# Performance work log

Measured on AMD Instinct MI355X. Metric: run time of the kernel, lower is better.

Reference implementation:

```python
import jax, jax.numpy as jnp
import numpy as np

N, C, A = 8192, 1000, 2048


def setup_inputs() -> dict:
    key = jax.random.key(0)
    k1, k2, k3, k4, k5, k6 = jax.random.split(key, 6)
    return {
        "fc": jax.random.normal(k1, (C, A), dtype=jnp.float32) * 0.02,
        "features_source": jax.random.normal(k2, (N, A), dtype=jnp.float32),
        "y_s": jax.random.normal(k3, (N, C), dtype=jnp.float32),
        "labels_source": jax.random.randint(k4, (N,), 0, C),
        "ratio": jnp.ones((1,), dtype=jnp.float32),
        "weights": jax.random.uniform(k5, (C,), dtype=jnp.float32, minval=0.5, maxval=1.5),
        "cv": jax.random.uniform(k6, (C, A), dtype=jnp.float32),
    }


def _metasaug_logits(fc, y_s, labels, cv, ratio):
    # sigma2[i,j] = ratio * sum_a (W[j,a] - W[y_i,a])^2 * cv[y_i,a]
    # expand the square -> three GEMM/reduction terms, avoiding the NxCxA tensor
    cv_y = cv[labels]            # (N, A)
    W_y = fc[labels]             # (N, A)
    term1 = cv_y @ (fc * fc).T                                   # (N, C)
    term2 = jnp.sum((W_y * W_y) * cv_y, axis=-1, keepdims=True)  # (N, 1)
    term3 = (W_y * cv_y) @ fc.T                                  # (N, C)
    sigma2 = ratio * (term1 + term2 - 2.0 * term3)
    return y_s + 0.5 * sigma2


def reference(fc, features_source, y_s, labels_source, ratio, weights, cv):
    # mode != 'update' path: augmented logits + class-weighted cross entropy
    aug_y = _metasaug_logits(fc, y_s, labels_source, cv, ratio)
    logp = jax.nn.log_softmax(aug_y, axis=-1)
    nll = -jnp.take_along_axis(logp, labels_source[:, None], axis=1)[:, 0]  # (N,)
    w = weights[labels_source]
    # torch weighted CE with mean reduction divides by sum of per-sample weights
    return jnp.sum(w * nll) / jnp.sum(w)
```

## Files before the change

### kernel.cpp

```cpp
#include <hip/hip_runtime.h>
#include <hip/hip_fp16.h>

#define N_SAMP 8192
#define C_CLS  1000
#define A_DIM  2048
#define KDIM   4096
#define CP     1024
#define ZSPLIT 8

typedef _Float16 half8 __attribute__((ext_vector_type(8)));
typedef _Float16 half4 __attribute__((ext_vector_type(4)));
typedef float    f32x4 __attribute__((ext_vector_type(4)));
typedef float    f32x16 __attribute__((ext_vector_type(16)));
typedef int      i32x4 __attribute__((ext_vector_type(4)));
typedef int      i32x8 __attribute__((ext_vector_type(8)));
typedef unsigned int u32x2 __attribute__((ext_vector_type(2)));

__global__ __launch_bounds__(256) void prep_kernel(const float* __restrict__ fc,
                                                   const float* __restrict__ cv,
                                                   unsigned char* __restrict__ Ab,
                                                   unsigned char* __restrict__ Bb) {
    int i4 = blockIdx.x * 256 + threadIdx.x;
    int c  = i4 >> 9;
    int k4 = i4 & 511;
    f32x4 f = {0.f, 0.f, 0.f, 0.f}, v = {0.f, 0.f, 0.f, 0.f};
    if (c < C_CLS) {
        size_t off = (size_t)c * (A_DIM / 4) + k4;
        f = ((const f32x4*)fc)[off];
        v = ((const f32x4*)cv)[off];
    }
    int alo = 0, ahi = 0, blo = 0, bhi = 0;
    alo = __builtin_amdgcn_cvt_pk_fp8_f32(v[0], v[1], alo, 0);
    alo = __builtin_amdgcn_cvt_pk_fp8_f32(v[2], v[3], alo, 1);
    ahi = __builtin_amdgcn_cvt_pk_fp8_f32(-32.f * f[0] * v[0], -32.f * f[1] * v[1], ahi, 0);
    ahi = __builtin_amdgcn_cvt_pk_fp8_f32(-32.f * f[2] * v[2], -32.f * f[3] * v[3], ahi, 1);
    blo = __builtin_amdgcn_cvt_pk_fp8_f32(256.f * f[0] * f[0], 256.f * f[1] * f[1], blo, 0);
    blo = __builtin_amdgcn_cvt_pk_fp8_f32(256.f * f[2] * f[2], 256.f * f[3] * f[3], blo, 1);
    bhi = __builtin_amdgcn_cvt_pk_fp8_f32(16.f * f[0], 16.f * f[1], bhi, 0);
    bhi = __builtin_amdgcn_cvt_pk_fp8_f32(16.f * f[2], 16.f * f[3], bhi, 1);
    size_t ro = (size_t)c * KDIM + k4 * 4;
    *(int*)(Ab + ro)         = alo;
    *(int*)(Ab + ro + A_DIM) = ahi;
    *(int*)(Bb + ro)         = blo;
    *(int*)(Bb + ro + A_DIM) = bhi;
}

template<int Z>
__global__ __launch_bounds__(256) void gemm_kernel(const unsigned char* __restrict__ A,
                                                   const unsigned char* __restrict__ B,
                                                   unsigned char* __restrict__ Spart) {
    constexpr int KS = KDIM / Z;
    constexpr int NT = KS / 64;
    __shared__ unsigned char As[2][128][64];
    __shared__ unsigned char Bs[2][128][64];

    const int z  = blockIdx.x;
    const int tj = blockIdx.y;
    const int tc = blockIdx.z;
    const int tid = threadIdx.x;
    const int lane = tid & 63;
    const int w  = tid >> 6;
    const int wr = w >> 1, wc = w & 1;
    const int k0 = z * KS;

    const size_t arow0 = (size_t)tc * 128;
    const size_t brow0 = (size_t)tj * 128;

#define STAGE(p, kcur)                                                                  \
    {                                                                                   \
        _Pragma("unroll")                                                               \
        for (int issue = 0; issue < 2; ++issue) {                                       \
            int t16 = issue * 256 + tid;                                                \
            int row = t16 >> 2, gp = t16 & 3;                                           \
            int gs  = gp ^ ((row >> 1) & 3);                                            \
            const unsigned char* ga = A + (arow0 + row) * KDIM + (kcur) + gs * 16;      \
            const unsigned char* gb = B + (brow0 + row) * KDIM + (kcur) + gs * 16;      \
            char* la = (char*)&As[p][0][0] + t16 * 16;                                  \
            char* lb = (char*)&Bs[p][0][0] + t16 * 16;                                  \
            __builtin_amdgcn_global_load_lds(                                           \
                (const __attribute__((address_space(1))) void*)ga,                      \
                (__attribute__((address_space(3))) void*)la, 16, 0, 0);                 \
            __builtin_amdgcn_global_load_lds(                                           \
                (const __attribute__((address_space(1))) void*)gb,                      \
                (__attribute__((address_space(3))) void*)lb, 16, 0, 0);                 \
        }                                                                               \
    }

    f32x16 acc[2][2] = {};
    const int r32   = lane & 31;
    const int khalf = lane >> 5;
    const int g0 = khalf * 2, g1 = khalf * 2 + 1;

    STAGE(0, k0);
    __syncthreads();
    for (int t = 0; t < NT; ++t) {
        int cur = t & 1;
        if (t + 1 < NT) STAGE(cur ^ 1, k0 + (t + 1) * 64);
        i32x8 af[2], bf[2];
        #pragma unroll
        for (int m = 0; m < 2; m++) {
            int row = wr * 64 + m * 32 + r32;
            int sw  = (row >> 1) & 3;
            i32x4 lo = *(const i32x4*)&As[cur][row][(g0 ^ sw) << 4];
            i32x4 hi = *(const i32x4*)&As[cur][row][(g1 ^ sw) << 4];
            af[m] = __builtin_shufflevector(lo, hi, 0, 1, 2, 3, 4, 5, 6, 7);
        }
        #pragma unroll
        for (int n = 0; n < 2; n++) {
            int row = wc * 64 + n * 32 + r32;
            int sw  = (row >> 1) & 3;
            i32x4 lo = *(const i32x4*)&Bs[cur][row][(g0 ^ sw) << 4];
            i32x4 hi = *(const i32x4*)&Bs[cur][row][(g1 ^ sw) << 4];
            bf[n] = __builtin_shufflevector(lo, hi, 0, 1, 2, 3, 4, 5, 6, 7);
        }
        #pragma unroll
        for (int m = 0; m < 2; m++)
            #pragma unroll
            for (int n = 0; n < 2; n++)
                acc[m][n] = __builtin_amdgcn_mfma_scale_f32_32x32x64_f8f6f4(
                    af[m], bf[n], acc[m][n], 0 , 0 ,
                    0, 127 , 0, 127 );
        __syncthreads();
    }
#undef STAGE

    unsigned char* Sp = Spart + (size_t)z * CP * CP;
    #pragma unroll
    for (int m = 0; m < 2; m++)
        #pragma unroll
        for (int n = 0; n < 2; n++)
            #pragma unroll
            for (int r = 0; r < 16; r++) {
                int orow = (r & 3) + 8 * (r >> 2) + 4 * khalf;
                int pk = __builtin_amdgcn_cvt_pk_fp8_f32(acc[m][n][r], acc[m][n][r], 0, 0);
                Sp[(size_t)(tc * 128 + wr * 64 + m * 32 + orow) * CP
                   + tj * 128 + wc * 64 + n * 32 + r32] = (unsigned char)(pk & 0xff);
            }
}

template<int Z>
__global__ __launch_bounds__(256) void ksum_kernel(const unsigned char* __restrict__ Spart,
                                                   _Float16* __restrict__ S) {
    size_t idx = (size_t)blockIdx.x * 256 + threadIdx.x;
    float a[8] = {};
    #pragma unroll
    for (int z = 0; z < Z; z++) {
        u32x2 v = *(const u32x2*)(Spart + (size_t)z * CP * CP + idx * 8);
        a[0] += __builtin_amdgcn_cvt_f32_fp8(v.x, 0);
        a[1] += __builtin_amdgcn_cvt_f32_fp8(v.x, 1);
        a[2] += __builtin_amdgcn_cvt_f32_fp8(v.x, 2);
        a[3] += __builtin_amdgcn_cvt_f32_fp8(v.x, 3);
        a[4] += __builtin_amdgcn_cvt_f32_fp8(v.y, 0);
        a[5] += __builtin_amdgcn_cvt_f32_fp8(v.y, 1);
        a[6] += __builtin_amdgcn_cvt_f32_fp8(v.y, 2);
        a[7] += __builtin_amdgcn_cvt_f32_fp8(v.y, 3);
    }
    half8 o;
    #pragma unroll
    for (int t = 0; t < 8; t++) o[t] = (_Float16)a[t];
    ((half8*)S)[idx] = o;
}

__global__ __launch_bounds__(256) void row_nll_kernel(const float* __restrict__ y_s,
                                                      const _Float16* __restrict__ S,
                                                      const int* __restrict__ labels,
                                                      const float* __restrict__ ratio,
                                                      const float* __restrict__ weights,
                                                      float* __restrict__ partial) {
    int lane = threadIdx.x & 63;
    int w = threadIdx.x >> 6;
    int i = blockIdx.x * 4 + w;
    int y = labels[i];
    float h = 0.5f * ratio[0] * (1.0f / 256.0f);
    const float*    ys_row = y_s + (size_t)i * C_CLS;
    const _Float16* s_row  = S   + (size_t)y * CP;

    float v[16];
    float m = -INFINITY;
    #pragma unroll
    for (int k = 0; k < 4; k++) {
        int j = lane * 4 + 256 * k;
        if (j < C_CLS) {
            f32x4 ys = *(const f32x4*)(ys_row + j);
            half4 sv = *(const half4*)(s_row + j);
            #pragma unroll
            for (int t = 0; t < 4; t++) {
                float val = ys[t] + h * (float)sv[t];
                v[k * 4 + t] = val;
                m = fmaxf(m, val);
            }
        } else {
            #pragma unroll
            for (int t = 0; t < 4; t++) v[k * 4 + t] = -INFINITY;
        }
    }
    #pragma unroll
    for (int off = 32; off; off >>= 1) m = fmaxf(m, __shfl_xor(m, off));
    float s = 0.f;
    #pragma unroll
    for (int k = 0; k < 16; k++) s += __expf(v[k] - m);
    #pragma unroll
    for (int off = 32; off; off >>= 1) s += __shfl_xor(s, off);

    __shared__ float swn[4], sww[4];
    if (lane == 0) {
        float target = ys_row[y] + h * (float)s_row[y];
        float wgt = weights[y];
        swn[w] = wgt * ((m + logf(s)) - target);
        sww[w] = wgt;
    }
    __syncthreads();
    if (threadIdx.x == 0) {
        partial[2 * blockIdx.x]     = swn[0] + swn[1] + swn[2] + swn[3];
        partial[2 * blockIdx.x + 1] = sww[0] + sww[1] + sww[2] + sww[3];
    }
}

#define NBLK_NLL (N_SAMP / 4)

__global__ __launch_bounds__(256) void finalize_kernel(const float* __restrict__ partial,
                                                       float* __restrict__ out) {
    float a = 0.f, b = 0.f;
    for (int i = threadIdx.x; i < NBLK_NLL; i += 256) {
        a += partial[2 * i];
        b += partial[2 * i + 1];
    }
    #pragma unroll
    for (int off = 32; off; off >>= 1) { a += __shfl_xor(a, off); b += __shfl_xor(b, off); }
    __shared__ float wa[4], wb[4];
    int w = threadIdx.x >> 6;
    if ((threadIdx.x & 63) == 0) { wa[w] = a; wb[w] = b; }
    __syncthreads();
    if (threadIdx.x == 0)
        out[0] = (wa[0] + wa[1] + wa[2] + wa[3]) / (wb[0] + wb[1] + wb[2] + wb[3]);
}

extern "C" void kernel_launch(void* const* d_in, const int* in_sizes, int n_in,
                              void* d_out, int out_size, void* d_ws, size_t ws_size,
                              hipStream_t stream) {
    const float* fc      = (const float*)d_in[0];
    const float* y_s     = (const float*)d_in[2];
    const int*   labels  = (const int*)d_in[3];
    const float* ratio   = (const float*)d_in[4];
    const float* weights = (const float*)d_in[5];
    const float* cv      = (const float*)d_in[6];

    char* ws = (char*)d_ws;
    unsigned char* Abuf  = (unsigned char*)ws;
    unsigned char* Bbuf  = (unsigned char*)(ws + (size_t)4 * 1024 * 1024);
    unsigned char* Spart = (unsigned char*)(ws + (size_t)8 * 1024 * 1024);
    _Float16*      S     = (_Float16*)(ws + (size_t)16 * 1024 * 1024);
    float*         part  = (float*)   (ws + (size_t)18 * 1024 * 1024);

    prep_kernel<<<(CP * A_DIM / 4) / 256, 256, 0, stream>>>(fc, cv, Abuf, Bbuf);
    gemm_kernel<ZSPLIT><<<dim3(ZSPLIT, 8, 8), 256, 0, stream>>>(Abuf, Bbuf, Spart);
    ksum_kernel<ZSPLIT><<<(CP * CP / 8) / 256, 256, 0, stream>>>(Spart, S);
    row_nll_kernel<<<NBLK_NLL, 256, 0, stream>>>(y_s, S, labels, ratio, weights, part);
    finalize_kernel<<<1, 256, 0, stream>>>(part, (float*)d_out);
}
```

Baseline: 35.91 us.

## Fuse split-K reduction into GEMM via intra-block per-wave K split and LDS sum

Replaces the grid-level split-K (8 z-slices writing fp8 partials to global memory, then a separate ksum kernel) with 64x64 output tiles, one 512-thread block per tile. Each of the 8 waves takes a K slice with its own private LDS double buffer and uses vmcnt waits instead of block barriers. At the end the waves' fp32 partials are summed through LDS and written as fp16. This removes a kernel launch, the fp8 partial round trip through global memory, and the fp8 quantization of the partials. In exchange it uses 128KB of LDS per block, so occupancy is one block per CU, and it relies on a vmcnt-only wait being enough for global_load_lds to finish before the wave reads LDS.

```diff
diff --git a/kernel.cpp b/kernel.cpp
--- a/kernel.cpp
+++ b/kernel.cpp
@@ -6,7 +6,6 @@
 #define A_DIM  2048
 #define KDIM   4096
 #define CP     1024
-#define ZSPLIT 8
 
 typedef _Float16 half8 __attribute__((ext_vector_type(8)));
 typedef _Float16 half4 __attribute__((ext_vector_type(4)));
@@ -14,7 +13,6 @@
 typedef float    f32x16 __attribute__((ext_vector_type(16)));
 typedef int      i32x4 __attribute__((ext_vector_type(4)));
 typedef int      i32x8 __attribute__((ext_vector_type(8)));
-typedef unsigned int u32x2 __attribute__((ext_vector_type(2)));
 
 __global__ __launch_bounds__(256) void prep_kernel(const float* __restrict__ fc,
                                                    const float* __restrict__ cv,
@@ -45,38 +43,32 @@
     *(int*)(Bb + ro + A_DIM) = bhi;
 }
 
-template<int Z>
-__global__ __launch_bounds__(256) void gemm_kernel(const unsigned char* __restrict__ A,
+__global__ __launch_bounds__(512) void gemm_kernel(const unsigned char* __restrict__ A,
                                                    const unsigned char* __restrict__ B,
-                                                   unsigned char* __restrict__ Spart) {
-    constexpr int KS = KDIM / Z;
-    constexpr int NT = KS / 64;
-    __shared__ unsigned char As[2][128][64];
-    __shared__ unsigned char Bs[2][128][64];
-
-    const int z  = blockIdx.x;
-    const int tj = blockIdx.y;
-    const int tc = blockIdx.z;
-    const int tid = threadIdx.x;
+                                                   _Float16* __restrict__ S) {
+    __shared__ __align__(16) unsigned char lds[8][16384];
+
+    const int tid  = threadIdx.x;
     const int lane = tid & 63;
-    const int w  = tid >> 6;
-    const int wr = w >> 1, wc = w & 1;
-    const int k0 = z * KS;
-
-    const size_t arow0 = (size_t)tc * 128;
-    const size_t brow0 = (size_t)tj * 128;
+    const int w    = tid >> 6;
+    const int bid  = blockIdx.x;
+    const int tc   = bid >> 4;
+    const int tj   = bid & 15;
+    const size_t arow0 = (size_t)tc * 64;
+    const size_t brow0 = (size_t)tj * 64;
+    const int kw = w * (KDIM / 8);
 
 #define STAGE(p, kcur)                                                                  \
     {                                                                                   \
         _Pragma("unroll")                                                               \
-        for (int issue = 0; issue < 2; ++issue) {                                       \
-            int t16 = issue * 256 + tid;                                                \
+        for (int s = 0; s < 4; ++s) {                                                   \
+            int t16 = s * 64 + lane;                                                    \
             int row = t16 >> 2, gp = t16 & 3;                                           \
             int gs  = gp ^ ((row >> 1) & 3);                                            \
             const unsigned char* ga = A + (arow0 + row) * KDIM + (kcur) + gs * 16;      \
             const unsigned char* gb = B + (brow0 + row) * KDIM + (kcur) + gs * 16;      \
-            char* la = (char*)&As[p][0][0] + t16 * 16;                                  \
-            char* lb = (char*)&Bs[p][0][0] + t16 * 16;                                  \
+            char* la = (char*)&lds[w][(p) * 8192 +        t16 * 16];                    \
+            char* lb = (char*)&lds[w][(p) * 8192 + 4096 + t16 * 16];                    \
             __builtin_amdgcn_global_load_lds(                                           \
                 (const __attribute__((address_space(1))) void*)ga,                      \
                 (__attribute__((address_space(3))) void*)la, 16, 0, 0);                 \
@@ -91,26 +83,30 @@
     const int khalf = lane >> 5;
     const int g0 = khalf * 2, g1 = khalf * 2 + 1;
 
-    STAGE(0, k0);
-    __syncthreads();
-    for (int t = 0; t < NT; ++t) {
-        int cur = t & 1;
-        if (t + 1 < NT) STAGE(cur ^ 1, k0 + (t + 1) * 64);
+    STAGE(0, kw);
+    for (int t = 0; t < 8; ++t) {
+        const int cur = t & 1;
+        if (t + 1 < 8) {
+            STAGE(cur ^ 1, kw + (t + 1) * 64);
+            asm volatile("s_waitcnt vmcnt(8)" ::: "memory");
+        } else {
+            asm volatile("s_waitcnt vmcnt(0)" ::: "memory");
+        }
         i32x8 af[2], bf[2];
         #pragma unroll
         for (int m = 0; m < 2; m++) {
-            int row = wr * 64 + m * 32 + r32;
+            int row = m * 32 + r32;
             int sw  = (row >> 1) & 3;
-            i32x4 lo = *(const i32x4*)&As[cur][row][(g0 ^ sw) << 4];
-            i32x4 hi = *(const i32x4*)&As[cur][row][(g1 ^ sw) << 4];
+            i32x4 lo = *(const i32x4*)&lds[w][cur * 8192 + row * 64 + ((g0 ^ sw) << 4)];
+            i32x4 hi = *(const i32x4*)&lds[w][cur * 8192 + row * 64 + ((g1 ^ sw) << 4)];
             af[m] = __builtin_shufflevector(lo, hi, 0, 1, 2, 3, 4, 5, 6, 7);
         }
         #pragma unroll
         for (int n = 0; n < 2; n++) {
-            int row = wc * 64 + n * 32 + r32;
+            int row = n * 32 + r32;
             int sw  = (row >> 1) & 3;
-            i32x4 lo = *(const i32x4*)&Bs[cur][row][(g0 ^ sw) << 4];
-            i32x4 hi = *(const i32x4*)&Bs[cur][row][(g1 ^ sw) << 4];
+            i32x4 lo = *(const i32x4*)&lds[w][cur * 8192 + 4096 + row * 64 + ((g0 ^ sw) << 4)];
+            i32x4 hi = *(const i32x4*)&lds[w][cur * 8192 + 4096 + row * 64 + ((g1 ^ sw) << 4)];
             bf[n] = __builtin_shufflevector(lo, hi, 0, 1, 2, 3, 4, 5, 6, 7);
         }
         #pragma unroll
@@ -120,45 +116,39 @@
                 acc[m][n] = __builtin_amdgcn_mfma_scale_f32_32x32x64_f8f6f4(
                     af[m], bf[n], acc[m][n], 0 , 0 ,
                     0, 127 , 0, 127 );
-        __syncthreads();
     }
 #undef STAGE
 
-    unsigned char* Sp = Spart + (size_t)z * CP * CP;
+    float* reg = (float*)&lds[w][0];
     #pragma unroll
     for (int m = 0; m < 2; m++)
         #pragma unroll
         for (int n = 0; n < 2; n++)
             #pragma unroll
             for (int r = 0; r < 16; r++) {
-                int orow = (r & 3) + 8 * (r >> 2) + 4 * khalf;
-                int pk = __builtin_amdgcn_cvt_pk_fp8_f32(acc[m][n][r], acc[m][n][r], 0, 0);
-                Sp[(size_t)(tc * 128 + wr * 64 + m * 32 + orow) * CP
-                   + tj * 128 + wc * 64 + n * 32 + r32] = (unsigned char)(pk & 0xff);
+                int row = m * 32 + (r & 3) + 8 * (r >> 2) + 4 * khalf;
+                int col = n * 32 + r32;
+                reg[row * 64 + col] = acc[m][n][r];
             }
-}
-
-template<int Z>
-__global__ __launch_bounds__(256) void ksum_kernel(const unsigned char* __restrict__ Spart,
-                                                   _Float16* __restrict__ S) {
-    size_t idx = (size_t)blockIdx.x * 256 + threadIdx.x;
-    float a[8] = {};
-    #pragma unroll
-    for (int z = 0; z < Z; z++) {
-        u32x2 v = *(const u32x2*)(Spart + (size_t)z * CP * CP + idx * 8);
-        a[0] += __builtin_amdgcn_cvt_f32_fp8(v.x, 0);
-        a[1] += __builtin_amdgcn_cvt_f32_fp8(v.x, 1);
-        a[2] += __builtin_amdgcn_cvt_f32_fp8(v.x, 2);
-        a[3] += __builtin_amdgcn_cvt_f32_fp8(v.x, 3);
-        a[4] += __builtin_amdgcn_cvt_f32_fp8(v.y, 0);
-        a[5] += __builtin_amdgcn_cvt_f32_fp8(v.y, 1);
-        a[6] += __builtin_amdgcn_cvt_f32_fp8(v.y, 2);
-        a[7] += __builtin_amdgcn_cvt_f32_fp8(v.y, 3);
-    }
-    half8 o;
-    #pragma unroll
-    for (int t = 0; t < 8; t++) o[t] = (_Float16)a[t];
-    ((half8*)S)[idx] = o;
+    __syncthreads();
+
+    {
+        const float* base = (const float*)&lds[0][0];
+        int e0 = tid * 8;
+        f32x4 s0 = {0.f, 0.f, 0.f, 0.f}, s1 = {0.f, 0.f, 0.f, 0.f};
+        #pragma unroll
+        for (int rgn = 0; rgn < 8; rgn++) {
+            const float* rb = base + rgn * 4096 + e0;
+            s0 += *(const f32x4*)rb;
+            s1 += *(const f32x4*)(rb + 4);
+        }
+        half8 o;
+        #pragma unroll
+        for (int q = 0; q < 4; q++) { o[q] = (_Float16)s0[q]; o[q + 4] = (_Float16)s1[q]; }
+        int orow = tid >> 3;
+        int ocol = (tid & 7) * 8;
+        *(half8*)&S[(size_t)(tc * 64 + orow) * CP + tj * 64 + ocol] = o;
+    }
 }
 
 __global__ __launch_bounds__(256) void row_nll_kernel(const float* __restrict__ y_s,
@@ -246,15 +236,13 @@
     const float* cv      = (const float*)d_in[6];
 
     char* ws = (char*)d_ws;
-    unsigned char* Abuf  = (unsigned char*)ws;
-    unsigned char* Bbuf  = (unsigned char*)(ws + (size_t)4 * 1024 * 1024);
-    unsigned char* Spart = (unsigned char*)(ws + (size_t)8 * 1024 * 1024);
-    _Float16*      S     = (_Float16*)(ws + (size_t)16 * 1024 * 1024);
-    float*         part  = (float*)   (ws + (size_t)18 * 1024 * 1024);
+    unsigned char* Abuf = (unsigned char*)ws;
+    unsigned char* Bbuf = (unsigned char*)(ws + (size_t)4 * 1024 * 1024);
+    _Float16*      S    = (_Float16*)(ws + (size_t)8 * 1024 * 1024);
+    float*         part = (float*)   (ws + (size_t)10 * 1024 * 1024);
 
     prep_kernel<<<(CP * A_DIM / 4) / 256, 256, 0, stream>>>(fc, cv, Abuf, Bbuf);
-    gemm_kernel<ZSPLIT><<<dim3(ZSPLIT, 8, 8), 256, 0, stream>>>(Abuf, Bbuf, Spart);
-    ksum_kernel<ZSPLIT><<<(CP * CP / 8) / 256, 256, 0, stream>>>(Spart, S);
+    gemm_kernel<<<256, 512, 0, stream>>>(Abuf, Bbuf, S);
     row_nll_kernel<<<NBLK_NLL, 256, 0, stream>>>(y_s, S, labels, ratio, weights, part);
     finalize_kernel<<<1, 256, 0, stream>>>(part, (float*)d_out);
 }
```

After: 37.31 us. 1.04x slower.
